# Kernel optimization log

Measured on AMD Instinct MI355X. Metric: run time of the kernel, lower is better.

Reference implementation:

```python
import jax, jax.numpy as jnp
import numpy as np

B, C, H, W = 4, 2048, 48, 48
D = 256  # hidden_channels


def setup_inputs() -> dict:
    key = jax.random.key(0)
    ks = jax.random.split(key, 6)
    return {
        "left_features": jax.random.normal(ks[0], (B, C, H, W), dtype=jnp.float32),
        "right_features": jax.random.normal(ks[1], (B, C, H, W), dtype=jnp.float32),
        "wq": jax.random.normal(ks[2], (D, C), dtype=jnp.float32) * 0.02,
        "bq": jax.random.normal(ks[3], (D,), dtype=jnp.float32) * 0.02,
        "wr": jax.random.normal(ks[4], (D, C), dtype=jnp.float32) * 0.02,
        "br": jax.random.normal(ks[5], (D,), dtype=jnp.float32) * 0.02,
    }


def _coattend(query, ref, wq, bq, wr, br):
    # 1x1 conv == per-pixel linear projection
    b, c, h, w = query.shape
    n = h * w
    q = jnp.einsum('bchw,dc->bhwd', query, wq) + bq     # [b,h,w,D]
    k = jnp.einsum('bchw,dc->bhwd', ref, wr) + br       # [b,h,w,D]
    qf = q.reshape(b, n, -1)                            # [b,n,D]
    kf = k.reshape(b, n, -1)                            # [b,n,D]
    scores = jnp.einsum('bnd,bmd->bnm', qf, kf)         # [b,n,n] (no sqrt(d) scaling, as in source)
    attn = jax.nn.softmax(scores, axis=-1)
    v = ref.reshape(b, c, n)                            # [b,c,n]
    out = jnp.einsum('bnm,bcm->bcn', attn, v)           # [b,c,n]
    return out.reshape(b, c, h, w)


def reference(left_features, right_features, wq, bq, wr, br):
    weighted_r = _coattend(left_features, right_features, wq, bq, wr, br)
    weighted_l = _coattend(right_features, left_features, wq, bq, wr, br)
    left_attended = jnp.concatenate([left_features, weighted_r], axis=1)   # [b,2c,h,w]
    right_attended = jnp.concatenate([right_features, weighted_l], axis=1)  # [b,2c,h,w]
    return (left_attended, right_attended)
```

## Files before the change

kernel.cpp:

```cpp
#include <hip/hip_runtime.h>

#define B_ 4
#define C_ 2048
#define N_ 2304
#define D_ 256

typedef _Float16 f16;
typedef __attribute__((ext_vector_type(8))) _Float16 f16x8;
typedef __attribute__((ext_vector_type(4))) _Float16 f16x4;
typedef __attribute__((ext_vector_type(4))) float    f32x4;

#define GLL(gp, dp)                                                        \
    __builtin_amdgcn_global_load_lds(                                      \
        (const __attribute__((address_space(1))) void*)(gp),               \
        (__attribute__((address_space(3))) void*)(dp), 16, 0, 0)

__global__ __launch_bounds__(256) void wsplit_kernel(
    const float* __restrict__ wq, const float* __restrict__ wr,
    f16* __restrict__ Wsp)
{
    const size_t WH = (size_t)D_ * C_;
    const size_t i4 = ((size_t)blockIdx.x * 256 + threadIdx.x) * 4;
    const float* src = (i4 < WH) ? (wq + i4) : (wr + (i4 - WH));
    const float4 x = *(const float4*)src;
    f16x4 h, lo;
    const float xs[4] = {x.x, x.y, x.z, x.w};
    #pragma unroll
    for (int i = 0; i < 4; ++i) {
        const f16 hh = (f16)xs[i];
        h[i] = hh; lo[i] = (f16)(xs[i] - (float)hh);
    }
    *(f16x4*)&Wsp[i4]          = h;
    *(f16x4*)&Wsp[2 * WH + i4] = lo;
}

__global__ __launch_bounds__(256, 2) void proj_mfma_kernel(
    const float* __restrict__ Xq, const float* __restrict__ Xr,
    const float* __restrict__ bq, const float* __restrict__ br,
    const f16* __restrict__ Wsp, f16* __restrict__ Qh, f16* __restrict__ Kh)
{
    __shared__ __align__(16) char smem[2][4][8192];
    char* const smbase = &smem[0][0][0];

    const int tid = threadIdx.x;
    const int w = tid >> 6, l = tid & 63;

    const int chunks = gridDim.x >> 3;
    const int bid = blockIdx.x;
    const int lin = (bid & 7) * chunks + (bid >> 3);
    const int qk = lin / 144;
    int rem = lin - qk * 144;
    const int b = rem / 36; rem -= b * 36;
    const int dt = rem / 18;
    const int nt = rem - dt * 18;
    const int n0 = nt * 128, d0 = dt * 128;

    const float* X    = qk ? Xr : Xq;
    const float* bias = qk ? br : bq;
    f16* Y  = qk ? Kh : Qh;
    f16* Yl = Y + (size_t)B_ * N_ * D_;

    const size_t WH = (size_t)D_ * C_;
    const f16* Wg0 = Wsp + (size_t)qk * WH + (size_t)((w >> 1) * 2) * WH;
    const int qb = (w & 1) * 4;
    const int srow   = l >> 2;
    const int schunk = (l & 3) ^ ((l >> 3) & 3);
    const char* gW = (const char*)Wg0
                   + ((size_t)(d0 + qb * 16 + srow)) * (C_ * 2) + schunk * 16;
    const size_t wrstep = (size_t)16 * C_ * 2;
    const int wtile = 2 + (w >> 1);

    const int cg = tid >> 5, ng = tid & 31;
    const float* Xb = X + (size_t)b * C_ * N_ + n0 + ng;
    const int awbase = ng * 64 + (((cg >> 1) ^ ((ng >> 1) & 3)) << 4) + ((cg & 1) << 3);

    const int wr_ = w >> 1, wc_ = w & 1;
    const int rc   = ((l >> 4) ^ ((l >> 1) & 3)) << 4;
    const int offA = (wr_ * 64 + (l & 15)) * 64 + rc;
    const int offB = (wc_ * 64 + (l & 15)) * 64 + rc;

    f32x4 acc[4][4] = {};

    #define WSTAGE(buf, s)                                                     \
        {                                                                      \
            const char* g_ = gW + (size_t)(s) * 64;                            \
            char* d_ = smbase + (buf) * 32768 + wtile * 8192 + qb * 1024;      \
            _Pragma("unroll")                                                  \
            for (int q = 0; q < 4; ++q) GLL(g_ + q * wrstep, d_ + q * 1024);   \
        }

    #define ALOAD(s, xv)                                                       \
        {                                                                      \
            _Pragma("unroll")                                                  \
            for (int r_ = 0; r_ < 4; ++r_) {                                   \
                const float* p_ = Xb + (size_t)((s) * 32 + cg * 4 + r_) * N_;  \
                _Pragma("unroll")                                              \
                for (int i_ = 0; i_ < 4; ++i_) xv[i_][r_] = p_[32 * i_];       \
            }                                                                  \
        }

    #define AWRITE(buf, xv)                                                    \
        {                                                                      \
            char* bb_ = smbase + (buf) * 32768;                                \
            _Pragma("unroll")                                                  \
            for (int i_ = 0; i_ < 4; ++i_) {                                   \
                f16x4 h_, lo_;                                                 \
                _Pragma("unroll")                                              \
                for (int r_ = 0; r_ < 4; ++r_) {                               \
                    const f16 hh_ = (f16)xv[i_][r_];                           \
                    h_[r_] = hh_; lo_[r_] = (f16)(xv[i_][r_] - (float)hh_);    \
                }                                                              \
                *(f16x4*)(bb_ +        awbase + i_ * 2048) = h_;               \
                *(f16x4*)(bb_ + 8192 + awbase + i_ * 2048) = lo_;              \
            }                                                                  \
        }

    {
        float xv[4][4];
        ALOAD(0, xv);
        WSTAGE(0, 0);
        AWRITE(0, xv);
    }
    __syncthreads();

    const int NSTEP = C_ / 32;
    for (int s = 0; s < NSTEP; ++s) {
        const int cur = s & 1;
        const bool more = (s + 1 < NSTEP);
        float nxv[4][4];
        if (more) {
            ALOAD(s + 1, nxv);
            WSTAGE(cur ^ 1, s + 1);
        }

        const char* t = smbase + cur * 32768;
        f16x8 ah[4], al[4], wh[4], wl[4];
        #pragma unroll
        for (int f = 0; f < 4; ++f) {
            ah[f] = *(const f16x8*)(t +         offA + f * 1024);
            al[f] = *(const f16x8*)(t +  8192 + offA + f * 1024);
            wh[f] = *(const f16x8*)(t + 16384 + offB + f * 1024);
            wl[f] = *(const f16x8*)(t + 24576 + offB + f * 1024);
        }
        #pragma unroll
        for (int i = 0; i < 4; ++i)
            #pragma unroll
            for (int j = 0; j < 4; ++j) {
                acc[i][j] = __builtin_amdgcn_mfma_f32_16x16x32_f16(ah[i], wh[j], acc[i][j], 0, 0, 0);
                acc[i][j] = __builtin_amdgcn_mfma_f32_16x16x32_f16(ah[i], wl[j], acc[i][j], 0, 0, 0);
                acc[i][j] = __builtin_amdgcn_mfma_f32_16x16x32_f16(al[i], wh[j], acc[i][j], 0, 0, 0);
            }

        if (more) AWRITE(cur ^ 1, nxv);
        __syncthreads();
    }
    #undef WSTAGE
    #undef ALOAD
    #undef AWRITE

    const int orow = n0 + wr_ * 64 + ((l >> 4) << 2);
    const int ocol = d0 + wc_ * 64 + (l & 15);
    float bb[4];
    #pragma unroll
    for (int j = 0; j < 4; ++j) bb[j] = bias[ocol + j * 16];
    #pragma unroll
    for (int i = 0; i < 4; ++i)
        #pragma unroll
        for (int j = 0; j < 4; ++j)
            #pragma unroll
            for (int p = 0; p < 4; ++p) {
                const float yv = acc[i][j][p] + bb[j];
                const f16 h = (f16)yv;
                const size_t idx = ((size_t)b * N_ + orow + i * 16 + p) * D_ + ocol + j * 16;
                Y[idx]  = h;
                Yl[idx] = (f16)(yv - (float)h);
            }
}

__global__ __launch_bounds__(256, 2) void scores_mfma_kernel(
    const f16* __restrict__ Qh, const f16* __restrict__ Kh,
    float* __restrict__ Sall)
{
    __shared__ __align__(16) char smem[2][4][8192];
    char* const smbase = &smem[0][0][0];

    const int tid = threadIdx.x;
    const int w = tid >> 6, l = tid & 63;

    const int chunks = gridDim.x >> 3;
    const int bid = blockIdx.x;
    const int lin = (bid & 7) * chunks + (bid >> 3);
    const int bl = lin / 324;
    const int rr = lin - bl * 324;
    const int mb = rr / 18;
    const int nb = rr - mb * 18;
    const int n0 = nb * 128, m0 = mb * 128;

    const size_t NQ = (size_t)B_ * N_ * D_;
    const int srow   = l >> 2;
    const int schunk = (l & 3) ^ ((l >> 3) & 3);
    const f16* tp = (w & 2) ? Kh : Qh;
    if (w & 1) tp += NQ;
    const int rbase = (w & 2) ? m0 : n0;
    const char* gT = (const char*)(tp + ((size_t)bl*N_ + rbase + srow)*D_) + schunk*16;
    const size_t rstep = (size_t)16 * D_ * 2;

    const int wr = w >> 1, wc = w & 1;
    const int rc   = ((l >> 4) ^ ((l >> 1) & 3)) << 4;
    const int offA = (wr * 64 + (l & 15)) * 64 + rc;
    const int offB = (wc * 64 + (l & 15)) * 64 + rc;

    f32x4 acc[4][4] = {};

    #define STAGES(buf, s)                                                 \
        {                                                                  \
            const char* g_ = gT + (size_t)(s) * 64;                        \
            char* d_ = smbase + (buf) * 32768 + w * 8192;                  \
            _Pragma("unroll")                                              \
            for (int q = 0; q < 8; ++q) GLL(g_ + q*rstep, d_ + q*1024);    \
        }

    STAGES(0, 0);
    __syncthreads();

    const int NSTEP = D_ / 32;
    for (int s = 0; s < NSTEP; ++s) {
        const int cur = s & 1;
        if (s + 1 < NSTEP) STAGES(cur ^ 1, s + 1);

        const char* t = smbase + cur * 32768;
        f16x8 qa0[4], qa1[4], kb0[4], kb1[4];
        #pragma unroll
        for (int f = 0; f < 4; ++f) {
            qa0[f] = *(const f16x8*)(t +         offA + f * 1024);
            qa1[f] = *(const f16x8*)(t +  8192 + offA + f * 1024);
            kb0[f] = *(const f16x8*)(t + 16384 + offB + f * 1024);
            kb1[f] = *(const f16x8*)(t + 24576 + offB + f * 1024);
        }
        #pragma unroll
        for (int i = 0; i < 4; ++i)
            #pragma unroll
            for (int j = 0; j < 4; ++j) {
                acc[i][j] = __builtin_amdgcn_mfma_f32_16x16x32_f16(qa0[i], kb0[j], acc[i][j], 0, 0, 0);
                acc[i][j] = __builtin_amdgcn_mfma_f32_16x16x32_f16(qa0[i], kb1[j], acc[i][j], 0, 0, 0);
                acc[i][j] = __builtin_amdgcn_mfma_f32_16x16x32_f16(qa1[i], kb0[j], acc[i][j], 0, 0, 0);
            }
        __syncthreads();
    }
    #undef STAGES

    float* Sb = Sall + (size_t)bl * N_ * N_;
    const int orow = n0 + wr * 64 + ((l >> 4) << 2);
    const int ocol = m0 + wc * 64 + (l & 15);
    #pragma unroll
    for (int i = 0; i < 4; ++i)
        #pragma unroll
        for (int j = 0; j < 4; ++j)
            #pragma unroll
            for (int p = 0; p < 4; ++p)
                Sb[(size_t)(orow + i*16 + p) * N_ + (ocol + j*16)] = acc[i][j][p];
}

__global__ __launch_bounds__(256) void softmax_kernel(float* __restrict__ S)
{
    const int tid = threadIdx.x;
    const int l = tid & 63;
    const size_t rowid = (size_t)blockIdx.x * 4 + (tid >> 6);
    float* row = S + rowid * N_;

    float v[36];
    float m = -3.4e38f;
    #pragma unroll
    for (int k = 0; k < 36; ++k) { v[k] = row[l + k*64]; m = fmaxf(m, v[k]); }
    #pragma unroll
    for (int off = 1; off < 64; off <<= 1) m = fmaxf(m, __shfl_xor(m, off));

    float sum = 0.f;
    #pragma unroll
    for (int k = 0; k < 36; ++k) { v[k] = __expf(v[k] - m); sum += v[k]; }
    #pragma unroll
    for (int off = 1; off < 64; off <<= 1) sum += __shfl_xor(sum, off);
    const float inv = 1.0f / sum;

    f16* rowh = (f16*)row;
    #pragma unroll
    for (int k = 0; k < 36; ++k) {
        const float p = v[k] * inv;
        const f16 hi = (f16)p;
        rowh[l + k*64]      = hi;
        rowh[N_ + l + k*64] = (f16)(p - (float)hi);
    }
}

__global__ __launch_bounds__(256, 3) void out_mfma_kernel(
    const float* __restrict__ Sall, const float* __restrict__ V,
    float* __restrict__ O)
{
    __shared__ __align__(16) char smem[2][3][8192];
    char* const smbase = &smem[0][0][0];

    const int tid = threadIdx.x;
    const int w = tid >> 6;
    const int l = tid & 63;

    const int chunks = gridDim.x >> 3;
    const int bid = blockIdx.x;
    const int lin = (bid & 7) * chunks + (bid >> 3);
    const int bl  = lin / 288;
    const int rr  = lin - bl * 288;
    const int cb  = rr / 18;
    const int nb  = rr - cb * 18;
    const int c0 = cb * 128, n0 = nb * 128;

    const int srow4  = l >> 2;
    const int schunk = (l & 3) ^ ((l >> 3) & 3);
    const char* Sb  = (const char*)Sall + (size_t)bl * N_ * N_ * 4;
    const char* gP0 = Sb + (size_t)(n0 + 2*w*16 + srow4) * ((size_t)N_ * 4) + schunk * 16;
    const char* gP1 = gP0 + (size_t)16 * N_ * 4;

    const int vr = tid >> 1;
    const int vc = (tid & 1) << 1;
    const float* Vg = V + ((size_t)bl * C_ + c0 + vr) * N_ + (vc << 3);
    const int vswz = (vr >> 1) & 3;
    const int wV0 = vr * 64 + ((vc    ) ^ vswz) * 16;
    const int wV1 = vr * 64 + ((vc + 1) ^ vswz) * 16;

    const int wr = w >> 1, wc = w & 1;
    const int rc   = ((l >> 4) ^ ((l >> 1) & 3)) << 4;
    const int offA = (wr * 64 + (l & 15)) * 64 + rc;
    const int offB = (wc * 64 + (l & 15)) * 64 + rc;

    f32x4 acc[4][4] = {};

    #define STAGEP(buf, s)                                                     \
        {                                                                      \
            const char* g0_ = gP0 + (size_t)(s) * 64;                          \
            const char* g1_ = gP1 + (size_t)(s) * 64;                          \
            char* dh_ = smbase + (buf) * 24576 + 8192 + 2 * w * 1024;          \
            char* dl_ = dh_ + 8192;                                            \
            GLL(g0_, dh_);           GLL(g0_ + 4608, dl_);                     \
            GLL(g1_, dh_ + 1024);    GLL(g1_ + 4608, dl_ + 1024);              \
        }

    #define VLOAD(s, x0, x1, x2, x3)                                           \
        {                                                                      \
            const float* vg_ = Vg + (size_t)(s) * 32;                          \
            x0 = *(const float4*)(vg_ + 0);  x1 = *(const float4*)(vg_ + 4);   \
            x2 = *(const float4*)(vg_ + 8);  x3 = *(const float4*)(vg_ + 12);  \
        }

    #define CVT8H(a, c, hi)                                                    \
        {                                                                      \
            const float xs_[8] = {a.x, a.y, a.z, a.w, c.x, c.y, c.z, c.w};     \
            _Pragma("unroll")                                                  \
            for (int i_ = 0; i_ < 8; ++i_) hi[i_] = (f16)xs_[i_];              \
        }

    #define VWRITE(buf, x0, x1, x2, x3)                                        \
        {                                                                      \
            f16x8 h0_, h1_;                                                    \
            CVT8H(x0, x1, h0_); CVT8H(x2, x3, h1_);                            \
            char* bb_ = smbase + (buf) * 24576;                                \
            *(f16x8*)(bb_ + wV0) = h0_;                                        \
            *(f16x8*)(bb_ + wV1) = h1_;                                        \
        }

    {
        float4 xa, xb, xc, xd;
        VLOAD(0, xa, xb, xc, xd);
        STAGEP(0, 0);
        VWRITE(0, xa, xb, xc, xd);
    }
    __syncthreads();

    const int NSTEP = N_ / 32;
    for (int s = 0; s < NSTEP; ++s) {
        const int cur = s & 1;
        const bool more = (s + 1 < NSTEP);
        float4 xa, xb, xc, xd;
        if (more) {
            VLOAD(s + 1, xa, xb, xc, xd);
            STAGEP(cur ^ 1, s + 1);
        }

        const char* t = smbase + cur * 24576;
        f16x8 va0[4], pb0[4], pb1[4];
        #pragma unroll
        for (int f = 0; f < 4; ++f) {
            va0[f] = *(const f16x8*)(t +         offA + f * 1024);
            pb0[f] = *(const f16x8*)(t +  8192 + offB + f * 1024);
            pb1[f] = *(const f16x8*)(t + 16384 + offB + f * 1024);
        }
        #pragma unroll
        for (int i = 0; i < 4; ++i)
            #pragma unroll
            for (int j = 0; j < 4; ++j) {
                acc[i][j] = __builtin_amdgcn_mfma_f32_16x16x32_f16(va0[i], pb0[j], acc[i][j], 0, 0, 0);
                acc[i][j] = __builtin_amdgcn_mfma_f32_16x16x32_f16(va0[i], pb1[j], acc[i][j], 0, 0, 0);
            }

        if (more) VWRITE(cur ^ 1, xa, xb, xc, xd);
        __syncthreads();
    }
    #undef STAGEP
    #undef VLOAD
    #undef CVT8H
    #undef VWRITE

    float* Ob = O + ((size_t)bl * (2 * C_) + C_) * N_;
    const int orow = c0 + wr * 64 + ((l >> 4) << 2);
    const int ocol = n0 + wc * 64 + (l & 15);
    #pragma unroll
    for (int i = 0; i < 4; ++i)
        #pragma unroll
        for (int j = 0; j < 4; ++j)
            #pragma unroll
            for (int p = 0; p < 4; ++p)
                Ob[(size_t)(orow + i * 16 + p) * N_ + (ocol + j * 16)] = acc[i][j][p];
}

__global__ __launch_bounds__(256) void copy_kernel(
    const float4* __restrict__ X, float4* __restrict__ O)
{
    const size_t perb = (size_t)C_ * N_ / 4;
    const size_t i = (size_t)blockIdx.x * 256 + threadIdx.x;
    const size_t b = i / perb, r = i - b * perb;
    O[b * 2 * perb + r] = X[i];
}

extern "C" void kernel_launch(void* const* d_in, const int* in_sizes, int n_in,
                              void* d_out, int out_size, void* d_ws, size_t ws_size,
                              hipStream_t stream)
{
    const float* left  = (const float*)d_in[0];
    const float* right = (const float*)d_in[1];
    const float* wq    = (const float*)d_in[2];
    const float* bq    = (const float*)d_in[3];
    const float* wr    = (const float*)d_in[4];
    const float* br    = (const float*)d_in[5];
    float* out = (float*)d_out;
    float* ws  = (float*)d_ws;

    const size_t QKn = (size_t)B_ * N_ * D_;

    f16*   Qh  = (f16*)ws;
    f16*   Kh  = (f16*)(ws + QKn);
    float* S   = ws + 2 * QKn;
    f16*   Wsp = (f16*)S;

    float* out1 = out;
    float* out2 = out + (size_t)B_ * 2 * C_ * N_;

    const dim3 blk(256);
    const int  gcopy = (B_ * C_ * N_ / 4) / 256;

    copy_kernel<<<gcopy, blk, 0, stream>>>((const float4*)left,  (float4*)out1);
    copy_kernel<<<gcopy, blk, 0, stream>>>((const float4*)right, (float4*)out2);

    wsplit_kernel<<<dim3(1024), blk, 0, stream>>>(wq, wr, Wsp);
    proj_mfma_kernel<<<dim3(288), blk, 0, stream>>>(left, right, bq, br, Wsp, Qh, Kh);
    scores_mfma_kernel<<<dim3(1296), blk, 0, stream>>>(Qh, Kh, S);
    softmax_kernel<<<dim3(2304), blk, 0, stream>>>(S);
    out_mfma_kernel<<<dim3(1152), blk, 0, stream>>>(S, right, out1);

    wsplit_kernel<<<dim3(1024), blk, 0, stream>>>(wq, wr, Wsp);
    proj_mfma_kernel<<<dim3(288), blk, 0, stream>>>(right, left, bq, br, Wsp, Qh, Kh);
    scores_mfma_kernel<<<dim3(1296), blk, 0, stream>>>(Qh, Kh, S);
    softmax_kernel<<<dim3(2304), blk, 0, stream>>>(S);
    out_mfma_kernel<<<dim3(1152), blk, 0, stream>>>(S, left, out2);
}
```

Baseline: 1.176 ms.

## Deepen out GEMM K-tile to 64 and merge the two concat copy launches

The attention-times-V GEMM now stages 64 columns of the reduction dimension per step instead of 32. It uses a new 128-byte-row XOR swizzle for both V and P tiles and a larger 64KB shared buffer, so occupancy drops to 2 blocks per CU. The intent is to halve the number of barriers and loop iterations and to issue wider loads per step, at the cost of more registers and LDS. It also appears to stage only the high fp16 half of the softmax output, where the old code also staged a low-residual half, which may reduce accuracy. Separately, the two concatenation copy kernels are fused into a single launch.

```diff
diff --git a/kernel.cpp b/kernel.cpp
--- a/kernel.cpp
+++ b/kernel.cpp
@@ -292,16 +292,15 @@
     }
 }
 
-__global__ __launch_bounds__(256, 3) void out_mfma_kernel(
+__global__ __launch_bounds__(256, 2) void out_mfma_kernel(
     const float* __restrict__ Sall, const float* __restrict__ V,
     float* __restrict__ O)
 {
-    __shared__ __align__(16) char smem[2][3][8192];
+    __shared__ __align__(16) char smem[2][2][16384];
     char* const smbase = &smem[0][0][0];
 
     const int tid = threadIdx.x;
-    const int w = tid >> 6;
-    const int l = tid & 63;
+    const int w = tid >> 6, l = tid & 63;
 
     const int chunks = gridDim.x >> 3;
     const int bid = blockIdx.x;
@@ -312,99 +311,106 @@
     const int nb  = rr - cb * 18;
     const int c0 = cb * 128, n0 = nb * 128;
 
-    const int srow4  = l >> 2;
-    const int schunk = (l & 3) ^ ((l >> 3) & 3);
-    const char* Sb  = (const char*)Sall + (size_t)bl * N_ * N_ * 4;
-    const char* gP0 = Sb + (size_t)(n0 + 2*w*16 + srow4) * ((size_t)N_ * 4) + schunk * 16;
-    const char* gP1 = gP0 + (size_t)16 * N_ * 4;
-
-    const int vr = tid >> 1;
-    const int vc = (tid & 1) << 1;
-    const float* Vg = V + ((size_t)bl * C_ + c0 + vr) * N_ + (vc << 3);
-    const int vswz = (vr >> 1) & 3;
-    const int wV0 = vr * 64 + ((vc    ) ^ vswz) * 16;
-    const int wV1 = vr * 64 + ((vc + 1) ^ vswz) * 16;
+    const int sc0 = (l & 7) ^ (l >> 4);
+    const int sc1 = sc0 ^ 4;
+    const char* Sb = (const char*)Sall + (size_t)bl * N_ * N_ * 4;
+    const size_t prs = (size_t)N_ * 4;
+    const char* gPa = Sb + (size_t)(n0 + 32*w     + (l >> 3)) * prs + sc0 * 16;
+    const char* gPb = Sb + (size_t)(n0 + 32*w + 8 + (l >> 3)) * prs + sc1 * 16;
+
+    const int vr = tid >> 1, vh = tid & 1;
+    const float* Vg = V + ((size_t)bl * C_ + c0 + vr) * N_ + vh * 32;
+    const int vx = (vr >> 1) & 7;
+    const int wVo0 = vr * 128 + (((vh << 2) + 0) ^ vx) * 16;
+    const int wVo1 = vr * 128 + (((vh << 2) + 1) ^ vx) * 16;
+    const int wVo2 = vr * 128 + (((vh << 2) + 2) ^ vx) * 16;
+    const int wVo3 = vr * 128 + (((vh << 2) + 3) ^ vx) * 16;
 
     const int wr = w >> 1, wc = w & 1;
-    const int rc   = ((l >> 4) ^ ((l >> 1) & 3)) << 4;
-    const int offA = (wr * 64 + (l & 15)) * 64 + rc;
-    const int offB = (wc * 64 + (l & 15)) * 64 + rc;
+    const int rxk = (l & 15) >> 1;
+    const int cA0 = (((l >> 4)    ) ^ rxk) << 4;
+    const int cA1 = (((l >> 4) + 4) ^ rxk) << 4;
+    const int rbaseA = (wr * 64 + (l & 15)) * 128;
+    const int rbaseB = (wc * 64 + (l & 15)) * 128;
 
     f32x4 acc[4][4] = {};
 
     #define STAGEP(buf, s)                                                     \
         {                                                                      \
-            const char* g0_ = gP0 + (size_t)(s) * 64;                          \
-            const char* g1_ = gP1 + (size_t)(s) * 64;                          \
-            char* dh_ = smbase + (buf) * 24576 + 8192 + 2 * w * 1024;          \
-            char* dl_ = dh_ + 8192;                                            \
-            GLL(g0_, dh_);           GLL(g0_ + 4608, dl_);                     \
-            GLL(g1_, dh_ + 1024);    GLL(g1_ + 4608, dl_ + 1024);              \
-        }
-
-    #define VLOAD(s, x0, x1, x2, x3)                                           \
-        {                                                                      \
-            const float* vg_ = Vg + (size_t)(s) * 32;                          \
-            x0 = *(const float4*)(vg_ + 0);  x1 = *(const float4*)(vg_ + 4);   \
-            x2 = *(const float4*)(vg_ + 8);  x3 = *(const float4*)(vg_ + 12);  \
-        }
-
-    #define CVT8H(a, c, hi)                                                    \
-        {                                                                      \
-            const float xs_[8] = {a.x, a.y, a.z, a.w, c.x, c.y, c.z, c.w};     \
+            const size_t so_ = (size_t)(s) * 128;                              \
+            char* d_ = smbase + (buf) * 32768 + 16384 + 4 * w * 1024;          \
+            GLL(gPa + so_,            d_);                                     \
+            GLL(gPb + so_,            d_ + 1024);                              \
+            GLL(gPa + so_ + 16*prs,   d_ + 2048);                              \
+            GLL(gPb + so_ + 16*prs,   d_ + 3072);                              \
+        }
+
+    #define VLOAD(s, xv)                                                       \
+        {                                                                      \
+            const float* vg_ = Vg + (size_t)(s) * 64;                          \
             _Pragma("unroll")                                                  \
-            for (int i_ = 0; i_ < 8; ++i_) hi[i_] = (f16)xs_[i_];              \
-        }
-
-    #define VWRITE(buf, x0, x1, x2, x3)                                        \
-        {                                                                      \
-            f16x8 h0_, h1_;                                                    \
-            CVT8H(x0, x1, h0_); CVT8H(x2, x3, h1_);                            \
-            char* bb_ = smbase + (buf) * 24576;                                \
-            *(f16x8*)(bb_ + wV0) = h0_;                                        \
-            *(f16x8*)(bb_ + wV1) = h1_;                                        \
+            for (int k_ = 0; k_ < 8; ++k_)                                     \
+                xv[k_] = *(const float4*)(vg_ + 4 * k_);                       \
+        }
+
+    #define VWRITE(buf, xv)                                                    \
+        {                                                                      \
+            char* bb_ = smbase + (buf) * 32768;                                \
+            f16x8 hv_[4];                                                      \
+            _Pragma("unroll")                                                  \
+            for (int k_ = 0; k_ < 4; ++k_) {                                   \
+                const float4 a_ = xv[2*k_], c_ = xv[2*k_ + 1];                 \
+                const float xs_[8] = {a_.x,a_.y,a_.z,a_.w,c_.x,c_.y,c_.z,c_.w};\
+                _Pragma("unroll")                                              \
+                for (int i_ = 0; i_ < 8; ++i_) hv_[k_][i_] = (f16)xs_[i_];     \
+            }                                                                  \
+            *(f16x8*)(bb_ + wVo0) = hv_[0];                                    \
+            *(f16x8*)(bb_ + wVo1) = hv_[1];                                    \
+            *(f16x8*)(bb_ + wVo2) = hv_[2];                                    \
+            *(f16x8*)(bb_ + wVo3) = hv_[3];                                    \
         }
 
     {
-        float4 xa, xb, xc, xd;
-        VLOAD(0, xa, xb, xc, xd);
+        float4 xv[8];
+        VLOAD(0, xv);
         STAGEP(0, 0);
-        VWRITE(0, xa, xb, xc, xd);
+        VWRITE(0, xv);
     }
     __syncthreads();
 
-    const int NSTEP = N_ / 32;
+    const int NSTEP = N_ / 64;
     for (int s = 0; s < NSTEP; ++s) {
         const int cur = s & 1;
         const bool more = (s + 1 < NSTEP);
-        float4 xa, xb, xc, xd;
+        float4 xv[8];
         if (more) {
-            VLOAD(s + 1, xa, xb, xc, xd);
+            VLOAD(s + 1, xv);
             STAGEP(cur ^ 1, s + 1);
         }
 
-        const char* t = smbase + cur * 24576;
-        f16x8 va0[4], pb0[4], pb1[4];
+        const char* tV = smbase + cur * 32768;
+        const char* tP = tV + 16384;
+        f16x8 va[4][2], pb[4][2];
         #pragma unroll
         for (int f = 0; f < 4; ++f) {
-            va0[f] = *(const f16x8*)(t +         offA + f * 1024);
-            pb0[f] = *(const f16x8*)(t +  8192 + offB + f * 1024);
-            pb1[f] = *(const f16x8*)(t + 16384 + offB + f * 1024);
+            va[f][0] = *(const f16x8*)(tV + rbaseA + f * 2048 + cA0);
+            va[f][1] = *(const f16x8*)(tV + rbaseA + f * 2048 + cA1);
+            pb[f][0] = *(const f16x8*)(tP + rbaseB + f * 2048 + cA0);
+            pb[f][1] = *(const f16x8*)(tP + rbaseB + f * 2048 + cA1);
         }
         #pragma unroll
         for (int i = 0; i < 4; ++i)
             #pragma unroll
             for (int j = 0; j < 4; ++j) {
-                acc[i][j] = __builtin_amdgcn_mfma_f32_16x16x32_f16(va0[i], pb0[j], acc[i][j], 0, 0, 0);
-                acc[i][j] = __builtin_amdgcn_mfma_f32_16x16x32_f16(va0[i], pb1[j], acc[i][j], 0, 0, 0);
+                acc[i][j] = __builtin_amdgcn_mfma_f32_16x16x32_f16(va[i][0], pb[j][0], acc[i][j], 0, 0, 0);
+                acc[i][j] = __builtin_amdgcn_mfma_f32_16x16x32_f16(va[i][1], pb[j][1], acc[i][j], 0, 0, 0);
             }
 
-        if (more) VWRITE(cur ^ 1, xa, xb, xc, xd);
+        if (more) VWRITE(cur ^ 1, xv);
         __syncthreads();
     }
     #undef STAGEP
     #undef VLOAD
-    #undef CVT8H
     #undef VWRITE
 
     float* Ob = O + ((size_t)bl * (2 * C_) + C_) * N_;
@@ -420,12 +426,17 @@
 }
 
 __global__ __launch_bounds__(256) void copy_kernel(
-    const float4* __restrict__ X, float4* __restrict__ O)
+    const float4* __restrict__ X1, const float4* __restrict__ X2,
+    float4* __restrict__ O)
 {
     const size_t perb = (size_t)C_ * N_ / 4;
-    const size_t i = (size_t)blockIdx.x * 256 + threadIdx.x;
+    const size_t tot = (size_t)B_ * perb;
+    size_t i = (size_t)blockIdx.x * 256 + threadIdx.x;
+    const float4* X = X1;
+    float4* Od = O;
+    if (i >= tot) { i -= tot; X = X2; Od = O + 2 * tot; }
     const size_t b = i / perb, r = i - b * perb;
-    O[b * 2 * perb + r] = X[i];
+    Od[b * 2 * perb + r] = X[i];
 }
 
 extern "C" void kernel_launch(void* const* d_in, const int* in_sizes, int n_in,
@@ -452,10 +463,10 @@
     float* out2 = out + (size_t)B_ * 2 * C_ * N_;
 
     const dim3 blk(256);
-    const int  gcopy = (B_ * C_ * N_ / 4) / 256;
-
-    copy_kernel<<<gcopy, blk, 0, stream>>>((const float4*)left,  (float4*)out1);
-    copy_kernel<<<gcopy, blk, 0, stream>>>((const float4*)right, (float4*)out2);
+    const int  gcopy = 2 * (B_ * C_ * N_ / 4) / 256;
+
+    copy_kernel<<<gcopy, blk, 0, stream>>>(
+        (const float4*)left, (const float4*)right, (float4*)out);
 
     wsplit_kernel<<<dim3(1024), blk, 0, stream>>>(wq, wr, Wsp);
     proj_mfma_kernel<<<dim3(288), blk, 0, stream>>>(left, right, bq, br, Wsp, Qh, Kh);
```

Result: no change. 1.168 ms (-0.7%).

## Drop hi/lo split of attention probabilities and merge copy launches

Applied to the files above, without the earlier changes.

Softmax now writes only a single fp16 copy of each probability instead of a hi/lo residual pair, and the output GEMM consumes a single P tile per step. This halves P staging traffic, LDS use and MFMA count in the output kernel, and the occupancy hint rises from 3 to 4 blocks. The two passthrough copy kernels are also fused into one launch. The cost is lower precision in the attention weights, which may push the output error closer to tolerance.

```diff
diff --git a/kernel.cpp b/kernel.cpp
--- a/kernel.cpp
+++ b/kernel.cpp
@@ -284,24 +284,19 @@
 
     f16* rowh = (f16*)row;
     #pragma unroll
-    for (int k = 0; k < 36; ++k) {
-        const float p = v[k] * inv;
-        const f16 hi = (f16)p;
-        rowh[l + k*64]      = hi;
-        rowh[N_ + l + k*64] = (f16)(p - (float)hi);
-    }
-}
-
-__global__ __launch_bounds__(256, 3) void out_mfma_kernel(
+    for (int k = 0; k < 36; ++k)
+        rowh[l + k*64] = (f16)(v[k] * inv);
+}
+
+__global__ __launch_bounds__(256, 4) void out_mfma_kernel(
     const float* __restrict__ Sall, const float* __restrict__ V,
     float* __restrict__ O)
 {
-    __shared__ __align__(16) char smem[2][3][8192];
+    __shared__ __align__(16) char smem[2][2][8192];
     char* const smbase = &smem[0][0][0];
 
     const int tid = threadIdx.x;
-    const int w = tid >> 6;
-    const int l = tid & 63;
+    const int w = tid >> 6, l = tid & 63;
 
     const int chunks = gridDim.x >> 3;
     const int bid = blockIdx.x;
@@ -334,12 +329,9 @@
 
     #define STAGEP(buf, s)                                                     \
         {                                                                      \
-            const char* g0_ = gP0 + (size_t)(s) * 64;                          \
-            const char* g1_ = gP1 + (size_t)(s) * 64;                          \
-            char* dh_ = smbase + (buf) * 24576 + 8192 + 2 * w * 1024;          \
-            char* dl_ = dh_ + 8192;                                            \
-            GLL(g0_, dh_);           GLL(g0_ + 4608, dl_);                     \
-            GLL(g1_, dh_ + 1024);    GLL(g1_ + 4608, dl_ + 1024);              \
+            char* dh_ = smbase + (buf) * 16384 + 8192 + 2 * w * 1024;          \
+            GLL(gP0 + (size_t)(s) * 64, dh_);                                  \
+            GLL(gP1 + (size_t)(s) * 64, dh_ + 1024);                           \
         }
 
     #define VLOAD(s, x0, x1, x2, x3)                                           \
@@ -360,7 +352,7 @@
         {                                                                      \
             f16x8 h0_, h1_;                                                    \
             CVT8H(x0, x1, h0_); CVT8H(x2, x3, h1_);                            \
-            char* bb_ = smbase + (buf) * 24576;                                \
+            char* bb_ = smbase + (buf) * 16384;                                \
             *(f16x8*)(bb_ + wV0) = h0_;                                        \
             *(f16x8*)(bb_ + wV1) = h1_;                                        \
         }
@@ -383,21 +375,19 @@
             STAGEP(cur ^ 1, s + 1);
         }
 
-        const char* t = smbase + cur * 24576;
-        f16x8 va0[4], pb0[4], pb1[4];
+        const char* tV = smbase + cur * 16384;
+        const char* tP = tV + 8192;
+        f16x8 va[4], pb[4];
         #pragma unroll
         for (int f = 0; f < 4; ++f) {
-            va0[f] = *(const f16x8*)(t +         offA + f * 1024);
-            pb0[f] = *(const f16x8*)(t +  8192 + offB + f * 1024);
-            pb1[f] = *(const f16x8*)(t + 16384 + offB + f * 1024);
+            va[f] = *(const f16x8*)(tV + offA + f * 1024);
+            pb[f] = *(const f16x8*)(tP + offB + f * 1024);
         }
         #pragma unroll
         for (int i = 0; i < 4; ++i)
             #pragma unroll
-            for (int j = 0; j < 4; ++j) {
-                acc[i][j] = __builtin_amdgcn_mfma_f32_16x16x32_f16(va0[i], pb0[j], acc[i][j], 0, 0, 0);
-                acc[i][j] = __builtin_amdgcn_mfma_f32_16x16x32_f16(va0[i], pb1[j], acc[i][j], 0, 0, 0);
-            }
+            for (int j = 0; j < 4; ++j)
+                acc[i][j] = __builtin_amdgcn_mfma_f32_16x16x32_f16(va[i], pb[j], acc[i][j], 0, 0, 0);
 
         if (more) VWRITE(cur ^ 1, xa, xb, xc, xd);
         __syncthreads();
@@ -420,12 +410,17 @@
 }
 
 __global__ __launch_bounds__(256) void copy_kernel(
-    const float4* __restrict__ X, float4* __restrict__ O)
+    const float4* __restrict__ X1, const float4* __restrict__ X2,
+    float4* __restrict__ O)
 {
     const size_t perb = (size_t)C_ * N_ / 4;
-    const size_t i = (size_t)blockIdx.x * 256 + threadIdx.x;
+    const size_t tot = (size_t)B_ * perb;
+    size_t i = (size_t)blockIdx.x * 256 + threadIdx.x;
+    const float4* X = X1;
+    float4* Od = O;
+    if (i >= tot) { i -= tot; X = X2; Od = O + 2 * tot; }
     const size_t b = i / perb, r = i - b * perb;
-    O[b * 2 * perb + r] = X[i];
+    Od[b * 2 * perb + r] = X[i];
 }
 
 extern "C" void kernel_launch(void* const* d_in, const int* in_sizes, int n_in,
@@ -452,10 +447,10 @@
     float* out2 = out + (size_t)B_ * 2 * C_ * N_;
 
     const dim3 blk(256);
-    const int  gcopy = (B_ * C_ * N_ / 4) / 256;
-
-    copy_kernel<<<gcopy, blk, 0, stream>>>((const float4*)left,  (float4*)out1);
-    copy_kernel<<<gcopy, blk, 0, stream>>>((const float4*)right, (float4*)out2);
+    const int  gcopy = 2 * (B_ * C_ * N_ / 4) / 256;
+
+    copy_kernel<<<gcopy, blk, 0, stream>>>(
+        (const float4*)left, (const float4*)right, (float4*)out);
 
     wsplit_kernel<<<dim3(1024), blk, 0, stream>>>(wq, wr, Wsp);
     proj_mfma_kernel<<<dim3(288), blk, 0, stream>>>(left, right, bq, br, Wsp, Qh, Kh);
```

Measured after the change: 1.058 ms. 10.0% less time.
